# Kernel optimization log

Hardware: AMD Instinct MI355X
Metric: run time of the kernel (lower is better)

Reference implementation:

```python
import jax, jax.numpy as jnp
import numpy as np

HIDDEN_NUMS = 512  # 2H = 1024, 4H = 2048


def setup_inputs() -> dict:
    key = jax.random.key(0)
    k1, k2, k3 = jax.random.split(key, 3)
    B, S, T, H2 = 32, 1024, 64, 2 * HIDDEN_NUMS
    target_hidden_states = jax.random.normal(k1, (B, T, H2), dtype=jnp.float32)
    hidden_states = jax.random.normal(k2, (B, S, H2), dtype=jnp.float32)
    # original uses RandomUniform(-0.01, 0.01)
    trans_W = jax.random.uniform(k3, (4 * HIDDEN_NUMS, H2), dtype=jnp.float32, minval=-0.01, maxval=0.01)
    trans_b = jnp.zeros((H2,), dtype=jnp.float32)
    return {
        'target_hidden_states': target_hidden_states,
        'hidden_states': hidden_states,
        'trans_W': trans_W,
        'trans_b': trans_b,
    }


def reference(target_hidden_states, hidden_states, trans_W, trans_b):
    # Vectorized form of the per-timestep while_loop (no cross-step recurrence):
    # scores[b,s,t] = <hidden[b,s], target[b,t]>
    scores = jnp.einsum('bsd,btd->bst', hidden_states, target_hidden_states)
    attn = jax.nn.softmax(scores, axis=-1)                      # (B, S, T)
    ti = jnp.einsum('bst,btd->bsd', attn, target_hidden_states)  # (B, S, 2H)
    cat = jnp.concatenate([hidden_states, ti], axis=-1)         # (B, S, 4H)
    hi_new = jnp.tanh(jnp.einsum('bsf,fd->bsd', cat, trans_W) + trans_b)
    return hi_new + hidden_states  # lf_layer residual
```

## Files before the change

### kernel.cpp

```cpp
#include <hip/hip_runtime.h>
#include <hip/hip_bf16.h>

#define BB 32
#define SS 1024
#define TT 64
#define HD 1024
#define FF 2048
#define MM (BB*SS)

typedef __attribute__((ext_vector_type(4))) float f32x4;
typedef __attribute__((ext_vector_type(8))) short bf16x8;
typedef __attribute__((ext_vector_type(8))) unsigned short u16x8;

__device__ __forceinline__ unsigned short f2bf(float f) {
  __hip_bfloat16 h = __float2bfloat16(f);
  return __builtin_bit_cast(unsigned short, h);
}

__device__ __forceinline__ void gll16(const void* g, void* l) {
  __builtin_amdgcn_global_load_lds(
      (const __attribute__((address_space(1))) void*)g,
      (__attribute__((address_space(3))) void*)l, 16, 0, 0);
}

__global__ void cvt_bf16_kernel(const float* __restrict__ x,
                                unsigned short* __restrict__ y, int n4) {
  int stride = gridDim.x * blockDim.x;
  for (int i = blockIdx.x * blockDim.x + threadIdx.x; i < n4; i += stride) {
    float4 v = reinterpret_cast<const float4*>(x)[i];
    ushort4 o;
    o.x = f2bf(v.x); o.y = f2bf(v.y); o.z = f2bf(v.z); o.w = f2bf(v.w);
    reinterpret_cast<ushort4*>(y)[i] = o;
  }
}

__global__ void tcvt_kernel(const float* __restrict__ in,
                            unsigned short* __restrict__ out, int R, int C) {
  __shared__ float tile[32][33];
  const int c0 = blockIdx.x * 32, r0 = blockIdx.y * 32;
  const int tx = threadIdx.x, ty = threadIdx.y;
#pragma unroll
  for (int j = 0; j < 4; ++j)
    tile[ty + j * 8][tx] = in[(size_t)(r0 + ty + j * 8) * C + c0 + tx];
  __syncthreads();
#pragma unroll
  for (int j = 0; j < 4; ++j)
    out[(size_t)(c0 + ty + j * 8) * R + r0 + tx] = f2bf(tile[tx][ty + j * 8]);
}

__global__ __launch_bounds__(256) void u_kernel(
    const unsigned short* __restrict__ tgt_bf,
    const unsigned short* __restrict__ Wt_bf,
    unsigned short* __restrict__ Ut)
{
  const int tid = threadIdx.x;
  const int w = tid >> 6, l = tid & 63;
  const int lrow = l & 15, lk = l >> 4;
  const int nb = blockIdx.x * 64;
  const int b = blockIdx.y;

  const unsigned short* ap = tgt_bf + (size_t)b * TT * HD
                             + (size_t)(w * 16 + lrow) * HD + lk * 8;
  const unsigned short* wp = Wt_bf + (size_t)(nb + lrow) * FF + 1024 + lk * 8;

  f32x4 acc[4] = {};
  for (int kt = 0; kt < 32; ++kt) {
    const int kk = kt * 32;
    bf16x8 a = *reinterpret_cast<const bf16x8*>(ap + kk);
#pragma unroll
    for (int ct = 0; ct < 4; ++ct) {
      bf16x8 bb = *reinterpret_cast<const bf16x8*>(wp + (size_t)ct * 16 * FF + kk);
      acc[ct] = __builtin_amdgcn_mfma_f32_16x16x32_bf16(a, bb, acc[ct], 0, 0, 0);
    }
  }
  unsigned short* up = Ut + (size_t)b * HD * TT;
#pragma unroll
  for (int ct = 0; ct < 4; ++ct)
#pragma unroll
    for (int j = 0; j < 4; ++j)
      up[(size_t)(nb + ct * 16 + lrow) * TT + (w * 16 + lk * 4 + j)] = f2bf(acc[ct][j]);
}

__global__ __launch_bounds__(256) void attn_kernel(
    const unsigned short* __restrict__ hid_bf,
    const unsigned short* __restrict__ tgt_bf,
    unsigned short* __restrict__ P_bf)
{
  const int tid = threadIdx.x;
  const int w = tid >> 6, l = tid & 63;
  const int lrow = l & 15, lk = l >> 4;
  const int b = blockIdx.y;
  const int sbase = blockIdx.x * 64;
  const size_t hbase = ((size_t)b * SS + sbase) * HD;

  const int qrow = w * 16 + lrow;
  const unsigned short* qp = hid_bf + hbase + (size_t)qrow * HD + lk * 8;
  const unsigned short* kp = tgt_bf + (size_t)b * TT * HD + (size_t)lrow * HD + lk * 8;

  f32x4 accs[4] = {};
#pragma unroll 2
  for (int kt = 0; kt < 32; ++kt) {
    const int kk = kt * 32;
    bf16x8 a = *reinterpret_cast<const bf16x8*>(qp + kk);
#pragma unroll
    for (int ct = 0; ct < 4; ++ct) {
      bf16x8 bb = *reinterpret_cast<const bf16x8*>(kp + (size_t)ct * 16 * HD + kk);
      accs[ct] = __builtin_amdgcn_mfma_f32_16x16x32_bf16(a, bb, accs[ct], 0, 0, 0);
    }
  }

  float p[4][4];
#pragma unroll
  for (int j = 0; j < 4; ++j) {
    float mx = fmaxf(fmaxf(accs[0][j], accs[1][j]), fmaxf(accs[2][j], accs[3][j]));
#pragma unroll
    for (int d = 1; d < 16; d <<= 1) mx = fmaxf(mx, __shfl_xor(mx, d, 64));
    float sum = 0.f;
#pragma unroll
    for (int ct = 0; ct < 4; ++ct) { p[ct][j] = __expf(accs[ct][j] - mx); sum += p[ct][j]; }
#pragma unroll
    for (int d = 1; d < 16; d <<= 1) sum += __shfl_xor(sum, d, 64);
    float inv = 1.f / sum;
#pragma unroll
    for (int ct = 0; ct < 4; ++ct) p[ct][j] *= inv;
  }
#pragma unroll
  for (int j = 0; j < 4; ++j) {
    const size_t prow = ((size_t)b * SS + sbase + w * 16 + lk * 4 + j) * TT;
#pragma unroll
    for (int ct = 0; ct < 4; ++ct)
      P_bf[prow + ct * 16 + lrow] = f2bf(p[ct][j]);
  }
}


__global__ __launch_bounds__(512) void gemm_kernel(
    const unsigned short* __restrict__ hid_bf,
    const unsigned short* __restrict__ P_bf,
    const unsigned short* __restrict__ Wt_bf,
    const unsigned short* __restrict__ Ut,
    const float* __restrict__ bias,
    float* __restrict__ out)
{
  __shared__ unsigned short lds[65536];

  const int tid = threadIdx.x;
  const int w = tid >> 6, l = tid & 63;
  const int wm = w >> 2, wn = w & 3;
  const int lrow = l & 15, lk = l >> 4;

  const int orig = blockIdx.y * 4 + blockIdx.x;
  const int lid = (orig & 7) * 64 + (orig >> 3);
  const int nbase = (lid & 3) * 256;
  const int mbase = (lid >> 2) * 256;
  const int bidx = mbase >> 10;

  const int srow8 = w * 8 + (l >> 3);
  const int scol = ((l & 7) ^ (l >> 3)) << 3;

  const int ck0 = ((lk)     ^ (lrow & 7)) << 3;
  const int ck1 = ((4 + lk) ^ (lrow & 7)) << 3;

#define STAGE_A(s, bsel, h) do {                                               \
    const unsigned short* p_; size_t str_;                                     \
    if ((s) < 16) { p_ = hid_bf + (s) * 64; str_ = 1024; }                     \
    else          { p_ = P_bf;              str_ = 64;   }                     \
    _Pragma("unroll")                                                          \
    for (int rd_ = 0; rd_ < 2; ++rd_)                                          \
      gll16(p_ + (size_t)(mbase + (h) * 128 + rd_ * 64 + srow8) * str_ + scol, \
            lds + (bsel) * 32768 + (h) * 8192 + rd_ * 4096 + w * 512);         \
  } while (0)

#define STAGE_B(s, bsel, h) do {                                               \
    const unsigned short* p_; size_t str_;                                     \
    if ((s) < 16) { p_ = Wt_bf + (s) * 64;               str_ = 2048; }        \
    else          { p_ = Ut + (size_t)bidx * HD * TT;    str_ = 64;   }        \
    _Pragma("unroll")                                                          \
    for (int rd_ = 0; rd_ < 2; ++rd_)                                          \
      gll16(p_ + (size_t)(nbase + (h) * 128 + rd_ * 64 + srow8) * str_ + scol, \
            lds + (bsel) * 32768 + 16384 + (h) * 8192 + rd_ * 4096 + w * 512); \
  } while (0)

#define PH_MID do { __builtin_amdgcn_s_setprio(1); } while (0)
#define PH_END do {                                                            \
    __builtin_amdgcn_s_setprio(0);                                             \
    __builtin_amdgcn_sched_barrier(0);                                         \
    __builtin_amdgcn_s_barrier();                                              \
  } while (0)

  f32x4 acc[8][4] = {};
  bf16x8 aR[4][2], bR[4][2];

  STAGE_A(0, 0, 0); STAGE_A(0, 0, 1);
  STAGE_B(0, 0, 0); STAGE_B(0, 0, 1);
  STAGE_B(1, 1, 0); STAGE_B(1, 1, 1);
  asm volatile("s_waitcnt vmcnt(4)" ::: "memory");
  __builtin_amdgcn_sched_barrier(0);
  __builtin_amdgcn_s_barrier();

#define TILE(tt, c, last) do {                                                 \
    const int sa_ = ((tt) + 1 > 16) ? 16 : (tt) + 1;                           \
    const int sb_ = ((tt) + 2 > 16) ? 16 : (tt) + 2;                           \
    const int abase_ = (c) * 32768 + wm * 8192 + lrow * 64;                    \
    const int bbase_ = (c) * 32768 + 16384 + (wn >> 1) * 8192                  \
                       + ((wn & 1) * 64 + lrow) * 64;                          \
           \
    _Pragma("unroll")                                                          \
    for (int m_ = 0; m_ < 4; ++m_) {                                           \
      aR[m_][0] = *(const bf16x8*)(lds + abase_ + m_ * 1024 + ck0);            \
      aR[m_][1] = *(const bf16x8*)(lds + abase_ + m_ * 1024 + ck1);            \
    }                                                                          \
    _Pragma("unroll")                                                          \
    for (int n_ = 0; n_ < 2; ++n_) {                                           \
      bR[n_][0] = *(const bf16x8*)(lds + bbase_ + n_ * 1024 + ck0);            \
      bR[n_][1] = *(const bf16x8*)(lds + bbase_ + n_ * 1024 + ck1);            \
    }                                                                          \
    STAGE_A(sa_, 1 - (c), 0);                                                  \
    PH_MID;                                                                    \
    _Pragma("unroll")                                                          \
    for (int m_ = 0; m_ < 4; ++m_)                                             \
      _Pragma("unroll")                                                        \
      for (int n_ = 0; n_ < 2; ++n_) {                                         \
        acc[m_][n_] = __builtin_amdgcn_mfma_f32_16x16x32_bf16(                 \
            aR[m_][0], bR[n_][0], acc[m_][n_], 0, 0, 0);                       \
        acc[m_][n_] = __builtin_amdgcn_mfma_f32_16x16x32_bf16(                 \
            aR[m_][1], bR[n_][1], acc[m_][n_], 0, 0, 0);                       \
      }                                                                        \
    PH_END;                                                                    \
                    \
    _Pragma("unroll")                                                          \
    for (int n_ = 2; n_ < 4; ++n_) {                                           \
      bR[n_][0] = *(const bf16x8*)(lds + bbase_ + n_ * 1024 + ck0);            \
      bR[n_][1] = *(const bf16x8*)(lds + bbase_ + n_ * 1024 + ck1);            \
    }                                                                          \
    STAGE_A(sa_, 1 - (c), 1);                                                  \
    PH_MID;                                                                    \
    _Pragma("unroll")                                                          \
    for (int m_ = 0; m_ < 4; ++m_)                                             \
      _Pragma("unroll")                                                        \
      for (int n_ = 2; n_ < 4; ++n_) {                                         \
        acc[m_][n_] = __builtin_amdgcn_mfma_f32_16x16x32_bf16(                 \
            aR[m_][0], bR[n_][0], acc[m_][n_], 0, 0, 0);                       \
        acc[m_][n_] = __builtin_amdgcn_mfma_f32_16x16x32_bf16(                 \
            aR[m_][1], bR[n_][1], acc[m_][n_], 0, 0, 0);                       \
      }                                                                        \
    PH_END;                                                                    \
                    \
    _Pragma("unroll")                                                          \
    for (int m_ = 0; m_ < 4; ++m_) {                                           \
      aR[m_][0] = *(const bf16x8*)(lds + abase_ + (m_ + 4) * 1024 + ck0);      \
      aR[m_][1] = *(const bf16x8*)(lds + abase_ + (m_ + 4) * 1024 + ck1);      \
    }                                                                          \
    STAGE_B(sb_, (c), 0);                                                      \
    PH_MID;                                                                    \
    _Pragma("unroll")                                                          \
    for (int m_ = 0; m_ < 4; ++m_)                                             \
      _Pragma("unroll")                                                        \
      for (int n_ = 0; n_ < 2; ++n_) {                                         \
        acc[m_ + 4][n_] = __builtin_amdgcn_mfma_f32_16x16x32_bf16(             \
            aR[m_][0], bR[n_][0], acc[m_ + 4][n_], 0, 0, 0);                   \
        acc[m_ + 4][n_] = __builtin_amdgcn_mfma_f32_16x16x32_bf16(             \
            aR[m_][1], bR[n_][1], acc[m_ + 4][n_], 0, 0, 0);                   \
      }                                                                        \
    PH_END;                                                                    \
                      \
    STAGE_B(sb_, (c), 1);                                                      \
    PH_MID;                                                                    \
    _Pragma("unroll")                                                          \
    for (int m_ = 0; m_ < 4; ++m_)                                             \
      _Pragma("unroll")                                                        \
      for (int n_ = 2; n_ < 4; ++n_) {                                         \
        acc[m_ + 4][n_] = __builtin_amdgcn_mfma_f32_16x16x32_bf16(             \
            aR[m_][0], bR[n_][0], acc[m_ + 4][n_], 0, 0, 0);                   \
        acc[m_ + 4][n_] = __builtin_amdgcn_mfma_f32_16x16x32_bf16(             \
            aR[m_][1], bR[n_][1], acc[m_ + 4][n_], 0, 0, 0);                   \
      }                                                                        \
    __builtin_amdgcn_s_setprio(0);                                             \
    if (last) { asm volatile("s_waitcnt vmcnt(0)" ::: "memory"); }             \
    else      { asm volatile("s_waitcnt vmcnt(4)" ::: "memory"); }             \
    __builtin_amdgcn_sched_barrier(0);                                         \
    __builtin_amdgcn_s_barrier();                                              \
  } while (0)

  for (int tt = 0; tt < 16; tt += 2) {
    TILE(tt, 0, false);
    TILE(tt + 1, 1, false);
  }
  TILE(16, 0, true);
#undef TILE
#undef PH_MID
#undef PH_END
#undef STAGE_A
#undef STAGE_B

#pragma unroll
  for (int m = 0; m < 8; ++m) {
    const int row = mbase + wm * 128 + m * 16 + lk * 4;
#pragma unroll
    for (int n = 0; n < 4; ++n) {
      const int col = nbase + wn * 64 + n * 16 + lrow;
      const float bv = bias[col];
#pragma unroll
      for (int j = 0; j < 4; ++j) {
        float x = acc[m][n][j] + bv;
        float xc = fminf(fmaxf(x, -15.f), 15.f);
        float e2 = __expf(2.f * xc);
        float th = (e2 - 1.f) / (e2 + 1.f);
        size_t oi = (size_t)(row + j) * HD + col;
        unsigned int u = ((unsigned int)hid_bf[oi]) << 16;
        out[oi] = th + __builtin_bit_cast(float, u);
      }
    }
  }
}

extern "C" void kernel_launch(void* const* d_in, const int* in_sizes, int n_in,
                              void* d_out, int out_size, void* d_ws, size_t ws_size,
                              hipStream_t stream) {
  const float* tgt  = (const float*)d_in[0];
  const float* hid  = (const float*)d_in[1];
  const float* W    = (const float*)d_in[2];
  const float* bias = (const float*)d_in[3];
  float* out = (float*)d_out;

  char* ws = (char*)d_ws;
  unsigned short* hid_bf = (unsigned short*)(ws);
  unsigned short* tgt_bf = (unsigned short*)(ws + 67108864);
  unsigned short* Wt_bf  = (unsigned short*)(ws + 71303168);
  unsigned short* P_bf   = (unsigned short*)(ws + 75497472);
  unsigned short* Ut     = (unsigned short*)(ws + 79691776);

  cvt_bf16_kernel<<<2048, 256, 0, stream>>>(hid, hid_bf, (MM * HD) / 4);
  cvt_bf16_kernel<<<512, 256, 0, stream>>>(tgt, tgt_bf, (BB * TT * HD) / 4);
  tcvt_kernel<<<dim3(HD / 32, FF / 32), dim3(32, 8), 0, stream>>>(W, Wt_bf, FF, HD);
  u_kernel<<<dim3(HD / 64, BB), 256, 0, stream>>>(tgt_bf, Wt_bf, Ut);
  attn_kernel<<<dim3(SS / 64, BB), 256, 0, stream>>>(hid_bf, tgt_bf, P_bf);
  gemm_kernel<<<dim3(HD / 128 / 2, MM / 256), 512, 0, stream>>>(hid_bf, P_bf, Wt_bf, Ut, bias, out);
}
```

Measured before the change: 217.4 us.

## Fuse attention scores and softmax into the main GEMM kernel

Removes the separate attention kernel and the P buffer round trip to global memory. The main GEMM now streams target rows into an extra LDS region alongside the hidden tiles and accumulates the score MFMAs during the hidden×W K-loop. It then runs a cross-wave softmax through LDS and does a final K-step of P×U from LDS. In exchange, each of the four N-blocks per M-tile recomputes the scores redundantly. LDS use, register pressure and epilogue barriers also increase.

```diff
diff --git a/kernel.cpp b/kernel.cpp
--- a/kernel.cpp
+++ b/kernel.cpp
@@ -10,7 +10,6 @@
 
 typedef __attribute__((ext_vector_type(4))) float f32x4;
 typedef __attribute__((ext_vector_type(8))) short bf16x8;
-typedef __attribute__((ext_vector_type(8))) unsigned short u16x8;
 
 __device__ __forceinline__ unsigned short f2bf(float f) {
   __hip_bfloat16 h = __float2bfloat16(f);
@@ -81,68 +80,16 @@
       up[(size_t)(nb + ct * 16 + lrow) * TT + (w * 16 + lk * 4 + j)] = f2bf(acc[ct][j]);
 }
 
-__global__ __launch_bounds__(256) void attn_kernel(
+
+__global__ __launch_bounds__(512) void gemm_kernel(
     const unsigned short* __restrict__ hid_bf,
     const unsigned short* __restrict__ tgt_bf,
-    unsigned short* __restrict__ P_bf)
-{
-  const int tid = threadIdx.x;
-  const int w = tid >> 6, l = tid & 63;
-  const int lrow = l & 15, lk = l >> 4;
-  const int b = blockIdx.y;
-  const int sbase = blockIdx.x * 64;
-  const size_t hbase = ((size_t)b * SS + sbase) * HD;
-
-  const int qrow = w * 16 + lrow;
-  const unsigned short* qp = hid_bf + hbase + (size_t)qrow * HD + lk * 8;
-  const unsigned short* kp = tgt_bf + (size_t)b * TT * HD + (size_t)lrow * HD + lk * 8;
-
-  f32x4 accs[4] = {};
-#pragma unroll 2
-  for (int kt = 0; kt < 32; ++kt) {
-    const int kk = kt * 32;
-    bf16x8 a = *reinterpret_cast<const bf16x8*>(qp + kk);
-#pragma unroll
-    for (int ct = 0; ct < 4; ++ct) {
-      bf16x8 bb = *reinterpret_cast<const bf16x8*>(kp + (size_t)ct * 16 * HD + kk);
-      accs[ct] = __builtin_amdgcn_mfma_f32_16x16x32_bf16(a, bb, accs[ct], 0, 0, 0);
-    }
-  }
-
-  float p[4][4];
-#pragma unroll
-  for (int j = 0; j < 4; ++j) {
-    float mx = fmaxf(fmaxf(accs[0][j], accs[1][j]), fmaxf(accs[2][j], accs[3][j]));
-#pragma unroll
-    for (int d = 1; d < 16; d <<= 1) mx = fmaxf(mx, __shfl_xor(mx, d, 64));
-    float sum = 0.f;
-#pragma unroll
-    for (int ct = 0; ct < 4; ++ct) { p[ct][j] = __expf(accs[ct][j] - mx); sum += p[ct][j]; }
-#pragma unroll
-    for (int d = 1; d < 16; d <<= 1) sum += __shfl_xor(sum, d, 64);
-    float inv = 1.f / sum;
-#pragma unroll
-    for (int ct = 0; ct < 4; ++ct) p[ct][j] *= inv;
-  }
-#pragma unroll
-  for (int j = 0; j < 4; ++j) {
-    const size_t prow = ((size_t)b * SS + sbase + w * 16 + lk * 4 + j) * TT;
-#pragma unroll
-    for (int ct = 0; ct < 4; ++ct)
-      P_bf[prow + ct * 16 + lrow] = f2bf(p[ct][j]);
-  }
-}
-
-
-__global__ __launch_bounds__(512) void gemm_kernel(
-    const unsigned short* __restrict__ hid_bf,
-    const unsigned short* __restrict__ P_bf,
     const unsigned short* __restrict__ Wt_bf,
     const unsigned short* __restrict__ Ut,
     const float* __restrict__ bias,
     float* __restrict__ out)
 {
-  __shared__ unsigned short lds[65536];
+  __shared__ unsigned short lds[73728];
 
   const int tid = threadIdx.x;
   const int w = tid >> 6, l = tid & 63;
@@ -160,14 +107,14 @@
 
   const int ck0 = ((lk)     ^ (lrow & 7)) << 3;
   const int ck1 = ((4 + lk) ^ (lrow & 7)) << 3;
+  const int tcol = wn * 16 + lrow;
 
 #define STAGE_A(s, bsel, h) do {                                               \
-    const unsigned short* p_; size_t str_;                                     \
-    if ((s) < 16) { p_ = hid_bf + (s) * 64; str_ = 1024; }                     \
-    else          { p_ = P_bf;              str_ = 64;   }                     \
+    const int ss_ = ((s) > 15) ? 15 : (s);                                     \
+    const unsigned short* p_ = hid_bf + ss_ * 64;                              \
     _Pragma("unroll")                                                          \
     for (int rd_ = 0; rd_ < 2; ++rd_)                                          \
-      gll16(p_ + (size_t)(mbase + (h) * 128 + rd_ * 64 + srow8) * str_ + scol, \
+      gll16(p_ + (size_t)(mbase + (h) * 128 + rd_ * 64 + srow8) * 1024 + scol, \
             lds + (bsel) * 32768 + (h) * 8192 + rd_ * 4096 + w * 512);         \
   } while (0)
 
@@ -179,6 +126,13 @@
     for (int rd_ = 0; rd_ < 2; ++rd_)                                          \
       gll16(p_ + (size_t)(nbase + (h) * 128 + rd_ * 64 + srow8) * str_ + scol, \
             lds + (bsel) * 32768 + 16384 + (h) * 8192 + rd_ * 4096 + w * 512); \
+  } while (0)
+
+#define STAGE_T(s, bsel) do {                                                  \
+    const int ss_ = ((s) > 15) ? 15 : (s);                                     \
+    gll16(tgt_bf + (size_t)bidx * TT * HD + (size_t)srow8 * HD + ss_ * 64      \
+              + scol,                                                          \
+          lds + 65536 + (bsel) * 4096 + w * 512);                              \
   } while (0)
 
 #define PH_MID do { __builtin_amdgcn_s_setprio(1); } while (0)
@@ -189,9 +143,11 @@
   } while (0)
 
   f32x4 acc[8][4] = {};
-  bf16x8 aR[4][2], bR[4][2];
+  f32x4 acc_s[8] = {};
+  bf16x8 aR[4][2], bR[4][2], tR0, tR1;
 
   STAGE_A(0, 0, 0); STAGE_A(0, 0, 1);
+  STAGE_T(0, 0);
   STAGE_B(0, 0, 0); STAGE_B(0, 0, 1);
   STAGE_B(1, 1, 0); STAGE_B(1, 1, 1);
   asm volatile("s_waitcnt vmcnt(4)" ::: "memory");
@@ -199,12 +155,13 @@
   __builtin_amdgcn_s_barrier();
 
 #define TILE(tt, c, last) do {                                                 \
-    const int sa_ = ((tt) + 1 > 16) ? 16 : (tt) + 1;                           \
+    const int sa_ = (tt) + 1;                                                  \
     const int sb_ = ((tt) + 2 > 16) ? 16 : (tt) + 2;                           \
     const int abase_ = (c) * 32768 + wm * 8192 + lrow * 64;                    \
     const int bbase_ = (c) * 32768 + 16384 + (wn >> 1) * 8192                  \
                        + ((wn & 1) * 64 + lrow) * 64;                          \
-           \
+    const int tbase_ = 65536 + (c) * 4096 + tcol * 64;                         \
+         \
     _Pragma("unroll")                                                          \
     for (int m_ = 0; m_ < 4; ++m_) {                                           \
       aR[m_][0] = *(const bf16x8*)(lds + abase_ + m_ * 1024 + ck0);            \
@@ -215,6 +172,8 @@
       bR[n_][0] = *(const bf16x8*)(lds + bbase_ + n_ * 1024 + ck0);            \
       bR[n_][1] = *(const bf16x8*)(lds + bbase_ + n_ * 1024 + ck1);            \
     }                                                                          \
+    tR0 = *(const bf16x8*)(lds + tbase_ + ck0);                                \
+    tR1 = *(const bf16x8*)(lds + tbase_ + ck1);                                \
     STAGE_A(sa_, 1 - (c), 0);                                                  \
     PH_MID;                                                                    \
     _Pragma("unroll")                                                          \
@@ -226,14 +185,22 @@
         acc[m_][n_] = __builtin_amdgcn_mfma_f32_16x16x32_bf16(                 \
             aR[m_][1], bR[n_][1], acc[m_][n_], 0, 0, 0);                       \
       }                                                                        \
+    _Pragma("unroll")                                                          \
+    for (int m_ = 0; m_ < 4; ++m_) {                                           \
+      acc_s[m_] = __builtin_amdgcn_mfma_f32_16x16x32_bf16(                     \
+          aR[m_][0], tR0, acc_s[m_], 0, 0, 0);                                 \
+      acc_s[m_] = __builtin_amdgcn_mfma_f32_16x16x32_bf16(                     \
+          aR[m_][1], tR1, acc_s[m_], 0, 0, 0);                                 \
+    }                                                                          \
     PH_END;                                                                    \
-                    \
+             \
     _Pragma("unroll")                                                          \
     for (int n_ = 2; n_ < 4; ++n_) {                                           \
       bR[n_][0] = *(const bf16x8*)(lds + bbase_ + n_ * 1024 + ck0);            \
       bR[n_][1] = *(const bf16x8*)(lds + bbase_ + n_ * 1024 + ck1);            \
     }                                                                          \
     STAGE_A(sa_, 1 - (c), 1);                                                  \
+    STAGE_T(sa_, 1 - (c));                                                     \
     PH_MID;                                                                    \
     _Pragma("unroll")                                                          \
     for (int m_ = 0; m_ < 4; ++m_)                                             \
@@ -245,7 +212,7 @@
             aR[m_][1], bR[n_][1], acc[m_][n_], 0, 0, 0);                       \
       }                                                                        \
     PH_END;                                                                    \
-                    \
+          \
     _Pragma("unroll")                                                          \
     for (int m_ = 0; m_ < 4; ++m_) {                                           \
       aR[m_][0] = *(const bf16x8*)(lds + abase_ + (m_ + 4) * 1024 + ck0);      \
@@ -262,6 +229,13 @@
         acc[m_ + 4][n_] = __builtin_amdgcn_mfma_f32_16x16x32_bf16(             \
             aR[m_][1], bR[n_][1], acc[m_ + 4][n_], 0, 0, 0);                   \
       }                                                                        \
+    _Pragma("unroll")                                                          \
+    for (int m_ = 0; m_ < 4; ++m_) {                                           \
+      acc_s[m_ + 4] = __builtin_amdgcn_mfma_f32_16x16x32_bf16(                 \
+          aR[m_][0], tR0, acc_s[m_ + 4], 0, 0, 0);                             \
+      acc_s[m_ + 4] = __builtin_amdgcn_mfma_f32_16x16x32_bf16(                 \
+          aR[m_][1], tR1, acc_s[m_ + 4], 0, 0, 0);                             \
+    }                                                                          \
     PH_END;                                                                    \
                       \
     STAGE_B(sb_, (c), 1);                                                      \
@@ -284,14 +258,110 @@
 
   for (int tt = 0; tt < 16; tt += 2) {
     TILE(tt, 0, false);
-    TILE(tt + 1, 1, false);
-  }
-  TILE(16, 0, true);
+    TILE(tt + 1, 1, (tt + 1) == 15);
+  }
 #undef TILE
+#undef STAGE_A
+#undef STAGE_B
+#undef STAGE_T
 #undef PH_MID
 #undef PH_END
-#undef STAGE_A
-#undef STAGE_B
+
+  {
+    float* smax = (float*)&lds[49152];
+    float* ssum = smax + 1024;
+    float mx[8][4], p[8][4];
+#pragma unroll
+    for (int m = 0; m < 8; ++m)
+#pragma unroll
+      for (int j = 0; j < 4; ++j) {
+        float v = acc_s[m][j];
+#pragma unroll
+        for (int d = 1; d < 16; d <<= 1) v = fmaxf(v, __shfl_xor(v, d, 64));
+        mx[m][j] = v;
+      }
+    if (lrow == 0) {
+#pragma unroll
+      for (int m = 0; m < 8; ++m)
+#pragma unroll
+        for (int j = 0; j < 4; ++j)
+          smax[(wm * 4 + wn) * 128 + m * 16 + lk * 4 + j] = mx[m][j];
+    }
+    __syncthreads();
+#pragma unroll
+    for (int m = 0; m < 8; ++m)
+#pragma unroll
+      for (int j = 0; j < 4; ++j) {
+        const int r = m * 16 + lk * 4 + j;
+        float v = fmaxf(fmaxf(smax[(wm * 4 + 0) * 128 + r], smax[(wm * 4 + 1) * 128 + r]),
+                        fmaxf(smax[(wm * 4 + 2) * 128 + r], smax[(wm * 4 + 3) * 128 + r]));
+        float e = __expf(acc_s[m][j] - v);
+        p[m][j] = e;
+        float s = e;
+#pragma unroll
+        for (int d = 1; d < 16; d <<= 1) s += __shfl_xor(s, d, 64);
+        mx[m][j] = s;
+      }
+    __syncthreads();
+    if (lrow == 0) {
+#pragma unroll
+      for (int m = 0; m < 8; ++m)
+#pragma unroll
+        for (int j = 0; j < 4; ++j)
+          ssum[(wm * 4 + wn) * 128 + m * 16 + lk * 4 + j] = mx[m][j];
+    }
+    __syncthreads();
+#pragma unroll
+    for (int m = 0; m < 8; ++m)
+#pragma unroll
+      for (int j = 0; j < 4; ++j) {
+        const int r = m * 16 + lk * 4 + j;
+        float tot = ssum[(wm * 4 + 0) * 128 + r] + ssum[(wm * 4 + 1) * 128 + r] +
+                    ssum[(wm * 4 + 2) * 128 + r] + ssum[(wm * 4 + 3) * 128 + r];
+        float pv = p[m][j] / tot;
+        const int off = wm * 8192 + r * 64 + ((((tcol) >> 3) ^ (r & 7)) << 3) + (tcol & 7);
+        lds[off] = f2bf(pv);
+      }
+    __syncthreads();
+  }
+
+  {
+    const int abase_ = wm * 8192 + lrow * 64;
+    const int bbase_ = 16384 + (wn >> 1) * 8192 + ((wn & 1) * 64 + lrow) * 64;
+#pragma unroll
+    for (int m_ = 0; m_ < 4; ++m_) {
+      aR[m_][0] = *(const bf16x8*)(lds + abase_ + m_ * 1024 + ck0);
+      aR[m_][1] = *(const bf16x8*)(lds + abase_ + m_ * 1024 + ck1);
+    }
+#pragma unroll
+    for (int n_ = 0; n_ < 4; ++n_) {
+      bR[n_][0] = *(const bf16x8*)(lds + bbase_ + n_ * 1024 + ck0);
+      bR[n_][1] = *(const bf16x8*)(lds + bbase_ + n_ * 1024 + ck1);
+    }
+#pragma unroll
+    for (int m_ = 0; m_ < 4; ++m_)
+#pragma unroll
+      for (int n_ = 0; n_ < 4; ++n_) {
+        acc[m_][n_] = __builtin_amdgcn_mfma_f32_16x16x32_bf16(
+            aR[m_][0], bR[n_][0], acc[m_][n_], 0, 0, 0);
+        acc[m_][n_] = __builtin_amdgcn_mfma_f32_16x16x32_bf16(
+            aR[m_][1], bR[n_][1], acc[m_][n_], 0, 0, 0);
+      }
+#pragma unroll
+    for (int m_ = 0; m_ < 4; ++m_) {
+      aR[m_][0] = *(const bf16x8*)(lds + abase_ + (m_ + 4) * 1024 + ck0);
+      aR[m_][1] = *(const bf16x8*)(lds + abase_ + (m_ + 4) * 1024 + ck1);
+    }
+#pragma unroll
+    for (int m_ = 0; m_ < 4; ++m_)
+#pragma unroll
+      for (int n_ = 0; n_ < 4; ++n_) {
+        acc[m_ + 4][n_] = __builtin_amdgcn_mfma_f32_16x16x32_bf16(
+            aR[m_][0], bR[n_][0], acc[m_ + 4][n_], 0, 0, 0);
+        acc[m_ + 4][n_] = __builtin_amdgcn_mfma_f32_16x16x32_bf16(
+            aR[m_][1], bR[n_][1], acc[m_ + 4][n_], 0, 0, 0);
+      }
+  }
 
 #pragma unroll
   for (int m = 0; m < 8; ++m) {
@@ -327,13 +397,11 @@
   unsigned short* hid_bf = (unsigned short*)(ws);
   unsigned short* tgt_bf = (unsigned short*)(ws + 67108864);
   unsigned short* Wt_bf  = (unsigned short*)(ws + 71303168);
-  unsigned short* P_bf   = (unsigned short*)(ws + 75497472);
   unsigned short* Ut     = (unsigned short*)(ws + 79691776);
 
   cvt_bf16_kernel<<<2048, 256, 0, stream>>>(hid, hid_bf, (MM * HD) / 4);
   cvt_bf16_kernel<<<512, 256, 0, stream>>>(tgt, tgt_bf, (BB * TT * HD) / 4);
   tcvt_kernel<<<dim3(HD / 32, FF / 32), dim3(32, 8), 0, stream>>>(W, Wt_bf, FF, HD);
   u_kernel<<<dim3(HD / 64, BB), 256, 0, stream>>>(tgt_bf, Wt_bf, Ut);
-  attn_kernel<<<dim3(SS / 64, BB), 256, 0, stream>>>(hid_bf, tgt_bf, P_bf);
-  gemm_kernel<<<dim3(HD / 128 / 2, MM / 256), 512, 0, stream>>>(hid_bf, P_bf, Wt_bf, Ut, bias, out);
-}
+  gemm_kernel<<<dim3(HD / 128 / 2, MM / 256), 512, 0, stream>>>(hid_bf, tgt_bf, Wt_bf, Ut, bias, out);
+}
```

After: 463.9 us. 2.13x slower.
